# Kernel optimization log

Measured on AMD Instinct MI355X. Metric: run time of the kernel, lower is better.

Reference implementation:

```python
import jax, jax.numpy as jnp
import numpy as np
from functools import partial

V, BS, L, H, C = 50257, 1024, 6, 12, 768
HD = C // H

def _ln(x, w, b):
    mu = jnp.mean(x, axis=-1, keepdims=True)
    var = jnp.var(x, axis=-1, keepdims=True)
    return (x - mu) * jax.lax.rsqrt(var + 1e-5) * w + b

def setup_inputs() -> dict:
    key = jax.random.key(0)
    ks = jax.random.split(key, 12)
    s = 0.02
    inp = {
        "idx": jax.random.randint(ks[0], (4, 1024), 0, V, dtype=jnp.int32),
        "wte": jax.random.normal(ks[1], (V, C), jnp.float32) * s,
        "wpe": jax.random.normal(ks[2], (BS, C), jnp.float32) * s,
        # per-block stacked params; linear weights stored [in, out]
        "ln1_w": jnp.ones((L, C)), "ln1_b": jnp.zeros((L, C)),
        "attn_w": jax.random.normal(ks[3], (L, C, 3 * C), jnp.float32) * s,
        "attn_b": jnp.zeros((L, 3 * C)),
        "proj_w": jax.random.normal(ks[4], (L, C, C), jnp.float32) * s,
        "proj_b": jnp.zeros((L, C)),
        "ln2_w": jnp.ones((L, C)), "ln2_b": jnp.zeros((L, C)),
        "fc_w": jax.random.normal(ks[5], (L, C, 4 * C), jnp.float32) * s,
        "fc_b": jnp.zeros((L, 4 * C)),
        "fc2_w": jax.random.normal(ks[6], (L, 4 * C, C), jnp.float32) * s,
        "fc2_b": jnp.zeros((L, C)),
        "lnf_w": jnp.ones((C,)), "lnf_b": jnp.zeros((C,)),
    }
    return inp

def _forward(idx, wte, wpe, ln1_w, ln1_b, attn_w, attn_b, proj_w, proj_b,
             ln2_w, ln2_b, fc_w, fc_b, fc2_w, fc2_b, lnf_w, lnf_b):
    B, T = idx.shape
    x = wte[idx] + wpe[:T]  # [B,T,C]
    causal = jnp.tril(jnp.ones((T, T), bool))  # [T,T]
    scale = 1.0 / np.sqrt(HD)
    neg_inf = jnp.finfo(x.dtype).min

    def block(x, p):
        l1w, l1b, aw, ab, pw, pb, l2w, l2b, fw, fb, f2w, f2b = p
        h = _ln(x, l1w, l1b)
        qkv = h @ aw + ab  # [B,T,3C]
        q, k, v = jnp.split(qkv, 3, axis=-1)
        q = q.reshape(B, T, H, HD)
        k = k.reshape(B, T, H, HD)
        v = v.reshape(B, T, H, HD)
        att = jnp.einsum('bqhd,bkhd->bhqk', q, k) * scale
        att = jnp.where(causal, att, neg_inf)
        att = jax.nn.softmax(att, axis=-1)
        y = jnp.einsum('bhqk,bkhd->bqhd', att, v).reshape(B, T, C)
        x = x + y @ pw + pb
        h = _ln(x, l2w, l2b)
        h = jax.nn.gelu(h @ fw + fb, approximate=False)  # torch nn.GELU default = exact
        x = x + h @ f2w + f2b
        return x, None

    params = (ln1_w, ln1_b, attn_w, attn_b, proj_w, proj_b,
              ln2_w, ln2_b, fc_w, fc_b, fc2_w, fc2_b)
    x, _ = jax.lax.scan(block, x, params)
    x = _ln(x, lnf_w, lnf_b)
    logits = x @ wte.T  # tied lm_head, no bias
    return logits

def reference(idx, wte, wpe, ln1_w, ln1_b, attn_w, attn_b, proj_w, proj_b,
              ln2_w, ln2_b, fc_w, fc_b, fc2_w, fc2_b, lnf_w, lnf_b):
    return _forward(idx, wte, wpe, ln1_w, ln1_b, attn_w, attn_b, proj_w, proj_b,
                    ln2_w, ln2_b, fc_w, fc_b, fc2_w, fc2_b, lnf_w, lnf_b)
```

## Files before the change

kernel.cpp:

```cpp
#include <hip/hip_runtime.h>

#define BT     4096
#define CDIM   768
#define NLAYER 6
#define NHEAD  12
#define VREAL  50257
#define VPAD   50432

typedef __bf16 bf16x8 __attribute__((ext_vector_type(8)));
typedef float  f32x4  __attribute__((ext_vector_type(4)));

__device__ __forceinline__ unsigned short f2bf(float f) {
    unsigned int u = __builtin_bit_cast(unsigned int, f);
    u += 0x7fffu + ((u >> 16) & 1u);
    return (unsigned short)(u >> 16);
}

__device__ __forceinline__ void gload16(const unsigned short* g, unsigned short* l) {
    __builtin_amdgcn_global_load_lds(
        (const __attribute__((address_space(1))) unsigned int*)g,
        (__attribute__((address_space(3))) unsigned int*)l, 16, 0, 0);
}

__device__ __forceinline__ void swz_block(int &bx, int &by) {
    int gx = gridDim.x;
    int nwg = gx * gridDim.y;
    if ((nwg & 7) == 0) {
        int lin = by * gx + bx;
        int q = nwg >> 3;
        lin = (lin & 7) * q + (lin >> 3);
        bx = lin % gx;
        by = lin / gx;
    }
}

__global__ __launch_bounds__(256) void transpose_conv(
    const float* __restrict__ in, unsigned short* __restrict__ out, int K, int N)
{
    in  += (size_t)blockIdx.z * K * N;
    out += (size_t)blockIdx.z * K * N;
    __shared__ float t[32][33];
    int j0 = blockIdx.x * 32;
    int i0 = blockIdx.y * 32;
    int c = threadIdx.x;
    int r = threadIdx.y;
    #pragma unroll
    for (int rr = r; rr < 32; rr += 8)
        t[rr][c] = in[(size_t)(i0 + rr) * N + j0 + c];
    __syncthreads();
    #pragma unroll
    for (int rr = r; rr < 32; rr += 8)
        out[(size_t)(j0 + rr) * K + i0 + c] = f2bf(t[c][rr]);
}

__global__ __launch_bounds__(256) void wteconv(
    const float* __restrict__ wte, unsigned short* __restrict__ out)
{
    size_t e = ((size_t)blockIdx.x * 256 + threadIdx.x) * 4;
    int row = (int)(e / CDIM);
    int col = (int)(e % CDIM);
    ushort4 o;
    if (row < VREAL) {
        float4 v = *(const float4*)(wte + (size_t)row * CDIM + col);
        o.x = f2bf(v.x); o.y = f2bf(v.y); o.z = f2bf(v.z); o.w = f2bf(v.w);
    } else {
        o.x = 0; o.y = 0; o.z = 0; o.w = 0;
    }
    *(ushort4*)(out + e) = o;
}

__global__ __launch_bounds__(256) void embed_kernel(
    const int* __restrict__ idx, const float* __restrict__ wte,
    const float* __restrict__ wpe, float* __restrict__ x)
{
    int row = blockIdx.x;
    int t = row & 1023;
    int id = idx[row];
    const float* s = wte + (size_t)id * CDIM;
    const float* p = wpe + (size_t)t * CDIM;
    float* o = x + (size_t)row * CDIM;
    for (int c = threadIdx.x; c < CDIM; c += 256) o[c] = s[c] + p[c];
}

__global__ __launch_bounds__(256) void ln_kernel(
    const float* __restrict__ x, const float* __restrict__ w,
    const float* __restrict__ b, unsigned short* __restrict__ out)
{
    int row = blockIdx.x * 4 + (threadIdx.x >> 6);
    int lane = threadIdx.x & 63;
    const float* xp = x + (size_t)row * CDIM;
    float v[12];
    float s = 0.f, sq = 0.f;
    #pragma unroll
    for (int j = 0; j < 12; ++j) {
        float t = xp[j * 64 + lane];
        v[j] = t; s += t; sq += t * t;
    }
    #pragma unroll
    for (int o = 32; o > 0; o >>= 1) {
        s  += __shfl_xor(s, o, 64);
        sq += __shfl_xor(sq, o, 64);
    }
    float mu  = s * (1.f / CDIM);
    float var = sq * (1.f / CDIM) - mu * mu;
    float rs  = rsqrtf(var + 1e-5f);
    unsigned short* op = out + (size_t)row * CDIM;
    #pragma unroll
    for (int j = 0; j < 12; ++j) {
        int c = j * 64 + lane;
        op[c] = f2bf((v[j] - mu) * rs * w[c] + b[c]);
    }
}

template<int MODE>
__global__ __launch_bounds__(256) void gemm_kernel(
    const unsigned short* __restrict__ A, const unsigned short* __restrict__ Bt,
    const float* __restrict__ bias, const float* __restrict__ resid,
    float* __restrict__ outF, unsigned short* __restrict__ outB,
    unsigned short* __restrict__ qout, unsigned short* __restrict__ kout,
    unsigned short* __restrict__ vtout,
    int K, int Nout)
{
    __shared__ alignas(16) unsigned short As[4096];
    __shared__ alignas(16) unsigned short Bs[4096];
    const int tid  = threadIdx.x;
    const int wv   = tid >> 6;
    const int lane = tid & 63;
    const int m0 = blockIdx.x * 128;
    const int n0 = blockIdx.y * 128;
    const int wr = wv >> 1, wc = wv & 1;
    const int srow = lane >> 2;
    const int skk  = (lane & 3) * 8;
    const int fr = lane & 15;
    const int fk = (lane >> 4) * 8;

    f32x4 acc[4][4];
    #pragma unroll
    for (int i = 0; i < 4; ++i)
        #pragma unroll
        for (int j = 0; j < 4; ++j) acc[i][j] = f32x4{0.f, 0.f, 0.f, 0.f};

    for (int k0 = 0; k0 < K; k0 += 32) {
        #pragma unroll
        for (int j = 0; j < 2; ++j) {
            int row = j * 64 + wv * 16 + srow;
            gload16(A  + (size_t)(m0 + row) * K + k0 + skk, &As[j * 2048 + wv * 512]);
            gload16(Bt + (size_t)(n0 + row) * K + k0 + skk, &Bs[j * 2048 + wv * 512]);
        }
        __syncthreads();
        bf16x8 a[4], bb[4];
        #pragma unroll
        for (int m = 0; m < 4; ++m)
            a[m] = *(const bf16x8*)&As[(wr * 64 + m * 16 + fr) * 32 + fk];
        #pragma unroll
        for (int n = 0; n < 4; ++n)
            bb[n] = *(const bf16x8*)&Bs[(wc * 64 + n * 16 + fr) * 32 + fk];
        #pragma unroll
        for (int m = 0; m < 4; ++m)
            #pragma unroll
            for (int n = 0; n < 4; ++n)
                acc[m][n] = __builtin_amdgcn_mfma_f32_16x16x32_bf16(
                    a[m], bb[n], acc[m][n], 0, 0, 0);
        __syncthreads();
    }

    const int colb = n0 + wc * 64 + fr;
    const int rowb = m0 + wr * 64 + (lane >> 4) * 4;
    #pragma unroll
    for (int m = 0; m < 4; ++m) {
        #pragma unroll
        for (int n = 0; n < 4; ++n) {
            int col = colb + n * 16;
            int which = col / 768;
            int hh = (col - which * 768) >> 6;
            int dd = col & 63;
            #pragma unroll
            for (int r = 0; r < 4; ++r) {
                int row = rowb + m * 16 + r;
                float v = acc[m][n][r];
                if (MODE == 1) {
                    outF[(size_t)row * Nout + col] =
                        resid[(size_t)row * Nout + col] + v + bias[col];
                } else if (MODE == 2) {
                    float u = v + bias[col];
                    float g = 0.5f * u * (1.f + erff(u * 0.70710678118654752f));
                    outB[(size_t)row * Nout + col] = f2bf(g);
                } else if (MODE == 4) {
                    int bb2 = row >> 10, tt = row & 1023;
                    unsigned short val = f2bf(v + bias[col]);
                    if (which == 0)
                        qout[(((size_t)bb2 * NHEAD + hh) * 1024 + tt) * 64 + dd] = val;
                    else if (which == 1)
                        kout[(((size_t)bb2 * NHEAD + hh) * 1024 + tt) * 64 + dd] = val;
                    else
                        vtout[(((size_t)bb2 * NHEAD + hh) * 64 + dd) * 1024 + tt] = val;
                }
            }
        }
    }
}

__global__ __launch_bounds__(512, 4) void lmhead_kernel(
    const unsigned short* __restrict__ A, const unsigned short* __restrict__ Bt,
    float* __restrict__ outF)
{
    __shared__ alignas(16) unsigned short ldsA[2][8192];
    const int tid  = threadIdx.x;
    const int wid  = tid >> 6;
    const int lane = tid & 63;
    const int fr = lane & 15, fg = lane >> 4;
    int bx = blockIdx.x, by = blockIdx.y;
    swz_block(bx, by);
    const int m0 = blockIdx.z * 2048 + bx * 128;
    const int n0 = by * 256;

    const int sr  = tid >> 3;
    const int sks = ((tid & 7) * 8) ^ ((sr & 7) << 3);
    const int wbase = wid * 512;

    const unsigned short* Bw = Bt + (size_t)(n0 + wid * 32 + fr) * 768 + fg * 8;

    const int arow = fr * 64;
    const int swz0 = (fg * 8) ^ ((fr & 7) << 3);
    const int swz1 = (32 + fg * 8) ^ ((fr & 7) << 3);

    f32x4 acc[8][2];
    #pragma unroll
    for (int m = 0; m < 8; ++m)
        #pragma unroll
        for (int n = 0; n < 2; ++n) acc[m][n] = f32x4{0.f, 0.f, 0.f, 0.f};

    bf16x8 brE[2][2], brO[2][2];

#define LM_STAGE_A(t, buf)                                                    \
    {                                                                         \
        const int k0_ = (t) * 64;                                             \
        gload16(A + (size_t)(m0 +      sr) * 768 + k0_ + sks,                 \
                &ldsA[buf][wbase]);                                           \
        gload16(A + (size_t)(m0 + 64 + sr) * 768 + k0_ + sks,                 \
                &ldsA[buf][4096 + wbase]);                                    \
    }
#define LM_LOAD_B(t, br)                                                      \
    {                                                                         \
        const int k0_ = (t) * 64;                                             \
        br[0][0] = *(const bf16x8*)(Bw + k0_);                                \
        br[0][1] = *(const bf16x8*)(Bw + k0_ + 32);                           \
        br[1][0] = *(const bf16x8*)(Bw + (size_t)16 * 768 + k0_);             \
        br[1][1] = *(const bf16x8*)(Bw + (size_t)16 * 768 + k0_ + 32);        \
    }
#define LM_COMPUTE(buf, br)                                                   \
    {                                                                         \
        _Pragma("unroll")                                                     \
        for (int m = 0; m < 8; ++m) {                                         \
            bf16x8 a0 = *(const bf16x8*)&ldsA[buf][m * 1024 + arow + swz0];   \
            bf16x8 a1 = *(const bf16x8*)&ldsA[buf][m * 1024 + arow + swz1];   \
            acc[m][0] = __builtin_amdgcn_mfma_f32_16x16x32_bf16(a0, br[0][0], acc[m][0], 0, 0, 0); \
            acc[m][1] = __builtin_amdgcn_mfma_f32_16x16x32_bf16(a0, br[1][0], acc[m][1], 0, 0, 0); \
            acc[m][0] = __builtin_amdgcn_mfma_f32_16x16x32_bf16(a1, br[0][1], acc[m][0], 0, 0, 0); \
            acc[m][1] = __builtin_amdgcn_mfma_f32_16x16x32_bf16(a1, br[1][1], acc[m][1], 0, 0, 0); \
        }                                                                     \
    }

    LM_STAGE_A(0, 0);
    LM_LOAD_B(0, brE);

    #pragma unroll 1
    for (int tt = 0; tt < 12; tt += 2) {
        LM_STAGE_A(tt + 1, 1);
        LM_LOAD_B(tt + 1, brO);
        asm volatile("s_waitcnt vmcnt(6)" ::: "memory");
        __builtin_amdgcn_s_barrier();
        __builtin_amdgcn_s_setprio(1);
        LM_COMPUTE(0, brE);
        __builtin_amdgcn_s_setprio(0);
        asm volatile("s_waitcnt lgkmcnt(0)" ::: "memory");
        __builtin_amdgcn_sched_barrier(0);
        __builtin_amdgcn_s_barrier();
        if (tt + 2 < 12) {
            LM_STAGE_A(tt + 2, 0);
            LM_LOAD_B(tt + 2, brE);
            asm volatile("s_waitcnt vmcnt(6)" ::: "memory");
        } else {
            asm volatile("s_waitcnt vmcnt(0)" ::: "memory");
        }
        __builtin_amdgcn_s_barrier();
        __builtin_amdgcn_s_setprio(1);
        LM_COMPUTE(1, brO);
        __builtin_amdgcn_s_setprio(0);
        asm volatile("s_waitcnt lgkmcnt(0)" ::: "memory");
        __builtin_amdgcn_sched_barrier(0);
        __builtin_amdgcn_s_barrier();
    }
#undef LM_STAGE_A
#undef LM_LOAD_B
#undef LM_COMPUTE

    const int colb = n0 + wid * 32 + fr;
    const int rowb = m0 + fg * 4;
    #pragma unroll
    for (int m = 0; m < 8; ++m) {
        #pragma unroll
        for (int n = 0; n < 2; ++n) {
            int col = colb + n * 16;
            if (col < VREAL) {
                #pragma unroll
                for (int r = 0; r < 4; ++r) {
                    int row = rowb + m * 16 + r;
                    outF[(size_t)row * VREAL + col] = acc[m][n][r];
                }
            }
        }
    }
}

__global__ __launch_bounds__(256) void attn_mfma_kernel(
    const unsigned short* __restrict__ qb, const unsigned short* __restrict__ kb,
    const unsigned short* __restrict__ vtb, unsigned short* __restrict__ y)
{
    __shared__ alignas(16) unsigned short Ps[4][16][72];
    const int qt = 15 - blockIdx.x;
    const int h = blockIdx.y, b = blockIdx.z;
    const int w = threadIdx.x >> 6, lane = threadIdx.x & 63;
    const int fr = lane & 15;
    const int fg = lane >> 4;
    const size_t bh = (size_t)(b * NHEAD + h);
    const unsigned short* Qb = qb  + bh * 1024 * 64;
    const unsigned short* Kb = kb  + bh * 1024 * 64;
    const unsigned short* Vt = vtb + bh * 64 * 1024;
    const int q0 = qt * 64 + w * 16;

    bf16x8 aq[2];
    aq[0] = *(const bf16x8*)(Qb + (size_t)(q0 + fr) * 64 + fg * 8);
    aq[1] = *(const bf16x8*)(Qb + (size_t)(q0 + fr) * 64 + 32 + fg * 8);

    f32x4 o[4];
    #pragma unroll
    for (int c = 0; c < 4; ++c) o[c] = f32x4{0.f, 0.f, 0.f, 0.f};
    float m[4], l[4];
    #pragma unroll
    for (int r = 0; r < 4; ++r) { m[r] = -1e30f; l[r] = 0.f; }

    for (int kt = 0; kt <= qt; ++kt) {
        const unsigned short* Kt = Kb + (size_t)kt * 64 * 64;
        f32x4 s[4];
        #pragma unroll
        for (int c = 0; c < 4; ++c) {
            bf16x8 bk0 = *(const bf16x8*)(Kt + (size_t)(c * 16 + fr) * 64 + fg * 8);
            bf16x8 bk1 = *(const bf16x8*)(Kt + (size_t)(c * 16 + fr) * 64 + 32 + fg * 8);
            s[c] = f32x4{0.f, 0.f, 0.f, 0.f};
            s[c] = __builtin_amdgcn_mfma_f32_16x16x32_bf16(aq[0], bk0, s[c], 0, 0, 0);
            s[c] = __builtin_amdgcn_mfma_f32_16x16x32_bf16(aq[1], bk1, s[c], 0, 0, 0);
        }
        float sc[4][4];
        #pragma unroll
        for (int c = 0; c < 4; ++c)
            #pragma unroll
            for (int r = 0; r < 4; ++r) {
                float v = s[c][r] * 0.125f;
                if (kt == qt && (kt * 64 + c * 16 + fr) > (q0 + fg * 4 + r))
                    v = -1e30f;
                sc[c][r] = v;
            }
        #pragma unroll
        for (int r = 0; r < 4; ++r) {
            float tm = fmaxf(fmaxf(sc[0][r], sc[1][r]), fmaxf(sc[2][r], sc[3][r]));
            tm = fmaxf(tm, __shfl_xor(tm, 1, 64));
            tm = fmaxf(tm, __shfl_xor(tm, 2, 64));
            tm = fmaxf(tm, __shfl_xor(tm, 4, 64));
            tm = fmaxf(tm, __shfl_xor(tm, 8, 64));
            float mn = fmaxf(m[r], tm);
            float corr = __expf(m[r] - mn);
            m[r] = mn;
            float ps = 0.f;
            #pragma unroll
            for (int c = 0; c < 4; ++c) {
                float p = __expf(sc[c][r] - mn);
                sc[c][r] = p;
                ps += p;
            }
            ps += __shfl_xor(ps, 1, 64);
            ps += __shfl_xor(ps, 2, 64);
            ps += __shfl_xor(ps, 4, 64);
            ps += __shfl_xor(ps, 8, 64);
            l[r] = l[r] * corr + ps;
            #pragma unroll
            for (int c = 0; c < 4; ++c) o[c][r] *= corr;
            #pragma unroll
            for (int c = 0; c < 4; ++c)
                Ps[w][fg * 4 + r][c * 16 + fr] = f2bf(sc[c][r]);
        }
        asm volatile("s_waitcnt lgkmcnt(0)" ::: "memory");
        bf16x8 ap0 = *(const bf16x8*)&Ps[w][fr][fg * 8];
        bf16x8 ap1 = *(const bf16x8*)&Ps[w][fr][32 + fg * 8];
        #pragma unroll
        for (int c = 0; c < 4; ++c) {
            const unsigned short* vb = Vt + (size_t)(c * 16 + fr) * 1024 + kt * 64;
            bf16x8 bv0 = *(const bf16x8*)(vb + fg * 8);
            bf16x8 bv1 = *(const bf16x8*)(vb + 32 + fg * 8);
            o[c] = __builtin_amdgcn_mfma_f32_16x16x32_bf16(ap0, bv0, o[c], 0, 0, 0);
            o[c] = __builtin_amdgcn_mfma_f32_16x16x32_bf16(ap1, bv1, o[c], 0, 0, 0);
        }
        asm volatile("s_waitcnt lgkmcnt(0)" ::: "memory");
    }

    float inv[4];
    #pragma unroll
    for (int r = 0; r < 4; ++r) inv[r] = 1.f / l[r];
    #pragma unroll
    for (int c = 0; c < 4; ++c)
        #pragma unroll
        for (int r = 0; r < 4; ++r) {
            int q = q0 + fg * 4 + r;
            y[((size_t)(b * 1024 + q)) * CDIM + h * 64 + c * 16 + fr] =
                f2bf(o[c][r] * inv[r]);
        }
}

extern "C" void kernel_launch(void* const* d_in, const int* in_sizes, int n_in,
                              void* d_out, int out_size, void* d_ws, size_t ws_size,
                              hipStream_t stream) {
    (void)in_sizes; (void)n_in; (void)out_size; (void)ws_size;
    const int*   idx   = (const int*)  d_in[0];
    const float* wte   = (const float*)d_in[1];
    const float* wpe   = (const float*)d_in[2];
    const float* ln1w  = (const float*)d_in[3];
    const float* ln1b  = (const float*)d_in[4];
    const float* attnw = (const float*)d_in[5];
    const float* attnb = (const float*)d_in[6];
    const float* projw = (const float*)d_in[7];
    const float* projb = (const float*)d_in[8];
    const float* ln2w  = (const float*)d_in[9];
    const float* ln2b  = (const float*)d_in[10];
    const float* fcw   = (const float*)d_in[11];
    const float* fcb   = (const float*)d_in[12];
    const float* fc2w  = (const float*)d_in[13];
    const float* fc2b  = (const float*)d_in[14];
    const float* lnfw  = (const float*)d_in[15];
    const float* lnfb  = (const float*)d_in[16];
    float* out = (float*)d_out;

    char* ws = (char*)d_ws;
    size_t off = 0;
    auto alloc = [&](size_t bytes) {
        void* p = ws + off;
        off += (bytes + 255) & ~(size_t)255;
        return p;
    };
    float*          x      = (float*)         alloc((size_t)BT * CDIM * 4);
    unsigned short* hbuf   = (unsigned short*)alloc((size_t)BT * CDIM * 2);
    unsigned short* qbuf   = (unsigned short*)alloc((size_t)BT * CDIM * 2);
    unsigned short* kbuf   = (unsigned short*)alloc((size_t)BT * CDIM * 2);
    unsigned short* vtbuf  = (unsigned short*)alloc((size_t)BT * CDIM * 2);
    unsigned short* ybuf   = (unsigned short*)alloc((size_t)BT * CDIM * 2);
    unsigned short* fcact  = (unsigned short*)alloc((size_t)BT * 4 * CDIM * 2);
    unsigned short* wqkvT  = (unsigned short*)alloc((size_t)NLAYER * 3 * CDIM * CDIM * 2);
    unsigned short* wprojT = (unsigned short*)alloc((size_t)NLAYER * CDIM * CDIM * 2);
    unsigned short* wfcT   = (unsigned short*)alloc((size_t)NLAYER * 4 * CDIM * CDIM * 2);
    unsigned short* wfc2T  = (unsigned short*)alloc((size_t)NLAYER * 4 * CDIM * CDIM * 2);
    unsigned short* wteB   = (unsigned short*)alloc((size_t)VPAD * CDIM * 2);

    transpose_conv<<<dim3(3*CDIM/32,   CDIM/32, NLAYER), dim3(32,8), 0, stream>>>(attnw, wqkvT, CDIM, 3*CDIM);
    transpose_conv<<<dim3(  CDIM/32,   CDIM/32, NLAYER), dim3(32,8), 0, stream>>>(projw, wprojT, CDIM, CDIM);
    transpose_conv<<<dim3(4*CDIM/32,   CDIM/32, NLAYER), dim3(32,8), 0, stream>>>(fcw,  wfcT,  CDIM, 4*CDIM);
    transpose_conv<<<dim3(  CDIM/32, 4*CDIM/32, NLAYER), dim3(32,8), 0, stream>>>(fc2w, wfc2T, 4*CDIM, CDIM);
    wteconv<<<(VPAD * CDIM / 4) / 256, 256, 0, stream>>>(wte, wteB);
    embed_kernel<<<BT, 256, 0, stream>>>(idx, wte, wpe, x);

    for (int l = 0; l < NLAYER; ++l) {
        ln_kernel<<<BT/4, 256, 0, stream>>>(x, ln1w + l*CDIM, ln1b + l*CDIM, hbuf);
        gemm_kernel<4><<<dim3(BT/128, 3*CDIM/128), 256, 0, stream>>>(
            hbuf, wqkvT + (size_t)l*3*CDIM*CDIM, attnb + (size_t)l*3*CDIM,
            nullptr, nullptr, nullptr, qbuf, kbuf, vtbuf, CDIM, 3*CDIM);
        attn_mfma_kernel<<<dim3(16, NHEAD, 4), 256, 0, stream>>>(qbuf, kbuf, vtbuf, ybuf);
        gemm_kernel<1><<<dim3(BT/128, CDIM/128), 256, 0, stream>>>(
            ybuf, wprojT + (size_t)l*CDIM*CDIM, projb + (size_t)l*CDIM,
            x, x, nullptr, nullptr, nullptr, nullptr, CDIM, CDIM);
        ln_kernel<<<BT/4, 256, 0, stream>>>(x, ln2w + l*CDIM, ln2b + l*CDIM, hbuf);
        gemm_kernel<2><<<dim3(BT/128, 4*CDIM/128), 256, 0, stream>>>(
            hbuf, wfcT + (size_t)l*4*CDIM*CDIM, fcb + (size_t)l*4*CDIM,
            nullptr, nullptr, fcact, nullptr, nullptr, nullptr, CDIM, 4*CDIM);
        gemm_kernel<1><<<dim3(BT/128, CDIM/128), 256, 0, stream>>>(
            fcact, wfc2T + (size_t)l*4*CDIM*CDIM, fc2b + (size_t)l*CDIM,
            x, x, nullptr, nullptr, nullptr, nullptr, 4*CDIM, CDIM);
    }
    ln_kernel<<<BT/4, 256, 0, stream>>>(x, lnfw, lnfb, hbuf);
    lmhead_kernel<<<dim3(16, VPAD/256, 2), 512, 0, stream>>>(hbuf, wteB, out);
}
```

Baseline: 2.353 ms.

## Halve LM-head block to 4 waves, each computing 128x64 output tile

The LM-head GEMM block drops from 8 waves to 4. Each wave now covers 64 output columns instead of 32, so every A fragment read from LDS feeds four MFMA column tiles instead of two. The A staging loop issues four global-to-LDS loads per thread, and the vmcnt waits are adjusted to the larger number of loads in flight. The aim is less LDS read traffic per MFMA, at the cost of twice the accumulator and B registers per wave and fewer waves to hide latency.

Result: no change. 2.355 ms (+0.1%).

```diff
diff --git a/kernel.cpp b/kernel.cpp
--- a/kernel.cpp
+++ b/kernel.cpp
@@ -200,13 +200,13 @@
     }
 }
 
-__global__ __launch_bounds__(512, 4) void lmhead_kernel(
+__global__ __launch_bounds__(256, 2) void lmhead_kernel(
     const unsigned short* __restrict__ A, const unsigned short* __restrict__ Bt,
     float* __restrict__ outF)
 {
     __shared__ alignas(16) unsigned short ldsA[2][8192];
     const int tid  = threadIdx.x;
-    const int wid  = tid >> 6;
+    const int wv   = tid >> 6;
     const int lane = tid & 63;
     const int fr = lane & 15, fg = lane >> 4;
     int bx = blockIdx.x, by = blockIdx.y;
@@ -214,50 +214,50 @@
     const int m0 = blockIdx.z * 2048 + bx * 128;
     const int n0 = by * 256;
 
-    const int sr  = tid >> 3;
-    const int sks = ((tid & 7) * 8) ^ ((sr & 7) << 3);
-    const int wbase = wid * 512;
-
-    const unsigned short* Bw = Bt + (size_t)(n0 + wid * 32 + fr) * 768 + fg * 8;
-
-    const int arow = fr * 64;
+    const int srow = wv * 8 + (lane >> 3);
+    const int sks  = ((lane & 7) * 8) ^ ((lane >> 3) << 3);
+
+    const unsigned short* Bw = Bt + (size_t)(n0 + wv * 64 + fr) * 768 + fg * 8;
+
     const int swz0 = (fg * 8) ^ ((fr & 7) << 3);
     const int swz1 = (32 + fg * 8) ^ ((fr & 7) << 3);
 
-    f32x4 acc[8][2];
+    f32x4 acc[8][4];
     #pragma unroll
     for (int m = 0; m < 8; ++m)
         #pragma unroll
-        for (int n = 0; n < 2; ++n) acc[m][n] = f32x4{0.f, 0.f, 0.f, 0.f};
-
-    bf16x8 brE[2][2], brO[2][2];
+        for (int n = 0; n < 4; ++n) acc[m][n] = f32x4{0.f, 0.f, 0.f, 0.f};
+
+    bf16x8 brE[4][2], brO[4][2];
 
 #define LM_STAGE_A(t, buf)                                                    \
     {                                                                         \
         const int k0_ = (t) * 64;                                             \
-        gload16(A + (size_t)(m0 +      sr) * 768 + k0_ + sks,                 \
-                &ldsA[buf][wbase]);                                           \
-        gload16(A + (size_t)(m0 + 64 + sr) * 768 + k0_ + sks,                 \
-                &ldsA[buf][4096 + wbase]);                                    \
+        _Pragma("unroll")                                                     \
+        for (int j = 0; j < 4; ++j)                                           \
+            gload16(A + (size_t)(m0 + j * 32 + srow) * 768 + k0_ + sks,       \
+                    &ldsA[buf][j * 2048 + wv * 512]);                         \
     }
 #define LM_LOAD_B(t, br)                                                      \
     {                                                                         \
         const int k0_ = (t) * 64;                                             \
-        br[0][0] = *(const bf16x8*)(Bw + k0_);                                \
-        br[0][1] = *(const bf16x8*)(Bw + k0_ + 32);                           \
-        br[1][0] = *(const bf16x8*)(Bw + (size_t)16 * 768 + k0_);             \
-        br[1][1] = *(const bf16x8*)(Bw + (size_t)16 * 768 + k0_ + 32);        \
+        _Pragma("unroll")                                                     \
+        for (int nf = 0; nf < 4; ++nf) {                                      \
+            br[nf][0] = *(const bf16x8*)(Bw + (size_t)nf * 16 * 768 + k0_);   \
+            br[nf][1] = *(const bf16x8*)(Bw + (size_t)nf * 16 * 768 + k0_ + 32); \
+        }                                                                     \
     }
 #define LM_COMPUTE(buf, br)                                                   \
     {                                                                         \
         _Pragma("unroll")                                                     \
         for (int m = 0; m < 8; ++m) {                                         \
-            bf16x8 a0 = *(const bf16x8*)&ldsA[buf][m * 1024 + arow + swz0];   \
-            bf16x8 a1 = *(const bf16x8*)&ldsA[buf][m * 1024 + arow + swz1];   \
-            acc[m][0] = __builtin_amdgcn_mfma_f32_16x16x32_bf16(a0, br[0][0], acc[m][0], 0, 0, 0); \
-            acc[m][1] = __builtin_amdgcn_mfma_f32_16x16x32_bf16(a0, br[1][0], acc[m][1], 0, 0, 0); \
-            acc[m][0] = __builtin_amdgcn_mfma_f32_16x16x32_bf16(a1, br[0][1], acc[m][0], 0, 0, 0); \
-            acc[m][1] = __builtin_amdgcn_mfma_f32_16x16x32_bf16(a1, br[1][1], acc[m][1], 0, 0, 0); \
+            bf16x8 a0 = *(const bf16x8*)&ldsA[buf][(m * 16 + fr) * 64 + swz0];\
+            bf16x8 a1 = *(const bf16x8*)&ldsA[buf][(m * 16 + fr) * 64 + swz1];\
+            _Pragma("unroll")                                                 \
+            for (int nf = 0; nf < 4; ++nf) {                                  \
+                acc[m][nf] = __builtin_amdgcn_mfma_f32_16x16x32_bf16(a0, br[nf][0], acc[m][nf], 0, 0, 0); \
+                acc[m][nf] = __builtin_amdgcn_mfma_f32_16x16x32_bf16(a1, br[nf][1], acc[m][nf], 0, 0, 0); \
+            }                                                                 \
         }                                                                     \
     }
 
@@ -268,7 +268,7 @@
     for (int tt = 0; tt < 12; tt += 2) {
         LM_STAGE_A(tt + 1, 1);
         LM_LOAD_B(tt + 1, brO);
-        asm volatile("s_waitcnt vmcnt(6)" ::: "memory");
+        asm volatile("s_waitcnt vmcnt(12)" ::: "memory");
         __builtin_amdgcn_s_barrier();
         __builtin_amdgcn_s_setprio(1);
         LM_COMPUTE(0, brE);
@@ -279,7 +279,7 @@
         if (tt + 2 < 12) {
             LM_STAGE_A(tt + 2, 0);
             LM_LOAD_B(tt + 2, brE);
-            asm volatile("s_waitcnt vmcnt(6)" ::: "memory");
+            asm volatile("s_waitcnt vmcnt(12)" ::: "memory");
         } else {
             asm volatile("s_waitcnt vmcnt(0)" ::: "memory");
         }
@@ -295,12 +295,12 @@
 #undef LM_LOAD_B
 #undef LM_COMPUTE
 
-    const int colb = n0 + wid * 32 + fr;
+    const int colb = n0 + wv * 64 + fr;
     const int rowb = m0 + fg * 4;
     #pragma unroll
     for (int m = 0; m < 8; ++m) {
         #pragma unroll
-        for (int n = 0; n < 2; ++n) {
+        for (int n = 0; n < 4; ++n) {
             int col = colb + n * 16;
             if (col < VREAL) {
                 #pragma unroll
@@ -484,5 +484,5 @@
             x, x, nullptr, nullptr, nullptr, nullptr, 4*CDIM, CDIM);
     }
     ln_kernel<<<BT/4, 256, 0, stream>>>(x, lnfw, lnfb, hbuf);
-    lmhead_kernel<<<dim3(16, VPAD/256, 2), 512, 0, stream>>>(hbuf, wteB, out);
-}
+    lmhead_kernel<<<dim3(16, VPAD/256, 2), 256, 0, stream>>>(hbuf, wteB, out);
+}
```
